# Optimization experiments

Measured on AMD Instinct MI355X. Metric: run time of the kernel, lower is better.

Reference implementation:

```python
import jax, jax.numpy as jnp
import numpy as np

B, H, L, D, S = 4, 16, 4096, 64, 128

def setup_inputs() -> dict:
    key = jax.random.key(0)
    k1, k2 = jax.random.split(key)
    x = jax.random.normal(k1, (B, H, L, D), dtype=jnp.float32)
    c = jax.random.normal(k2, (H, S, D), dtype=jnp.float32)
    # codebook rows are unit-normalized at init (matches torch init)
    c = c / jnp.linalg.norm(c, axis=-1, keepdims=True)
    return {"x": x, "c": c}

def reference(x, c):
    # cosine-similarity scores: [B,H,L,S]
    cos_sim = jnp.einsum('bhld,hsd->bhls', x, c)
    delta_index = jnp.argmax(cos_sim, axis=-1)            # [B,H,L]
    delta_onehot = jax.nn.one_hot(delta_index, c.shape[-2], dtype=jnp.float32)  # [B,H,L,S]
    return (delta_onehot, c)
```

## Files before the change

### kernel.cpp

```cpp
#include <hip/hip_runtime.h>
#include <math.h>

constexpr int BB = 4;
constexpr int HH = 16;
constexpr int LL = 4096;
constexpr int DD = 64;
constexpr int SS = 128;
constexpr int BM = 128;
constexpr int GG = 2;

constexpr float TAU = 2e-3f;

typedef __attribute__((ext_vector_type(8))) short bf16x8;
typedef __attribute__((ext_vector_type(4))) float f32x4;

#define MFMA16 __builtin_amdgcn_mfma_f32_16x16x32_bf16

__device__ __forceinline__ unsigned short f2bf(float v) {
    unsigned u = __float_as_uint(v);
    return (unsigned short)((u + 0x7fffu + ((u >> 16) & 1u)) >> 16);
}

__device__ __forceinline__ void split8(const float4 va, const float4 vb,
                                       uint4* hi, uint4* lo) {
    const float v[8] = {va.x, va.y, va.z, va.w, vb.x, vb.y, vb.z, vb.w};
    unsigned hw[4], lw[4];
    #pragma unroll
    for (int p = 0; p < 4; ++p) {
        const unsigned u0 = __float_as_uint(v[2 * p]);
        const unsigned u1 = __float_as_uint(v[2 * p + 1]);
        const unsigned h0 = u0 & 0xffff0000u;
        const unsigned h1 = u1 & 0xffff0000u;
        hw[p] = (u0 >> 16) | h1;
        lw[p] = (unsigned)f2bf(v[2 * p] - __uint_as_float(h0))
              | ((unsigned)f2bf(v[2 * p + 1] - __uint_as_float(h1)) << 16);
    }
    *hi = make_uint4(hw[0], hw[1], hw[2], hw[3]);
    *lo = make_uint4(lw[0], lw[1], lw[2], lw[3]);
}

union FragU { uint4 q; bf16x8 v; };

__global__ __launch_bounds__(256) void convert_c_kernel(
    const float* __restrict__ c, unsigned char* __restrict__ ws,
    float* __restrict__ out_c)
{
    const int sid = blockIdx.x * 256 + threadIdx.x;
    const int h  = sid >> 10;
    const int r  = sid & 1023;
    const int kt = r >> 9;
    const int ct = (r >> 6) & 7;
    const int ln = r & 63;
    const int cc = ct * 16 + (ln & 15);
    const int k0 = kt * 32 + (ln >> 4) * 8;
    const float4* src = (const float4*)(c + ((size_t)h * SS + cc) * DD + k0);
    uint4 hi, lo;
    split8(src[0], src[1], &hi, &lo);
    unsigned char* base =
        ws + (size_t)h * 32768 + (size_t)(((kt << 3) | ct) * 1024 + ln * 16);
    *(uint4*)(base) = hi;
    *(uint4*)(base + 16384) = lo;

    const f32x4* __restrict__ s4 = (const f32x4*)c;
    f32x4* __restrict__ d4 = (f32x4*)out_c;
    __builtin_nontemporal_store(s4[sid], d4 + sid);
    __builtin_nontemporal_store(s4[sid + 16384], d4 + sid + 16384);
}

__device__ __forceinline__ void load_a(const float* __restrict__ x,
                                       long long rbase, int wv, int lane,
                                       float4* raw) {
    const int ln15 = lane & 15;
    const int k0 = (lane >> 4) * 8;
    #pragma unroll
    for (int rtb = 0; rtb < 2; ++rtb) {
        const float* xr =
            x + (size_t)(rbase + wv * 32 + rtb * 16 + ln15) * DD + k0;
        #pragma unroll
        for (int kt = 0; kt < 2; ++kt) {
            raw[rtb * 4 + kt * 2 + 0] = *(const float4*)(xr + kt * 32);
            raw[rtb * 4 + kt * 2 + 1] = *(const float4*)(xr + kt * 32 + 4);
        }
    }
}

__device__ __forceinline__ void split_a(const float4* raw, bf16x8 af[2][2][2]) {
    #pragma unroll
    for (int rtb = 0; rtb < 2; ++rtb)
        #pragma unroll
        for (int kt = 0; kt < 2; ++kt) {
            FragU hi, lo;
            split8(raw[rtb * 4 + kt * 2], raw[rtb * 4 + kt * 2 + 1],
                   &hi.q, &lo.q);
            af[rtb][kt][0] = hi.v;
            af[rtb][kt][1] = lo.v;
        }
}

template <bool USE_WS>
__global__ __launch_bounds__(256, 2) void quantizer_kernel(
    const float* __restrict__ x,
    const float* __restrict__ c,
    const unsigned char* __restrict__ ws,
    float* __restrict__ out,
    float* __restrict__ out_c)
{
    __shared__ __align__(16) unsigned char smemB[32768];
    __shared__ int amax[GG][BM];
    __shared__ int s_wcnt[4];
    __shared__ int s_wlist[4][32];

    const int tid = threadIdx.x;
    const int wv = tid >> 6;
    const int lane = tid & 63;
    const int ln15 = lane & 15;
    const int blk = blockIdx.x;
    const long long base0 = (long long)blk * (GG * BM);
    const int h = (int)((base0 >> 12) & (HH - 1));
    const float* __restrict__ chead = c + (size_t)h * SS * DD;

    if (USE_WS) {
        const unsigned char* wsb = ws + (size_t)h * 32768;
        #pragma unroll
        for (int it = 0; it < 8; ++it) {
            const unsigned off = (unsigned)(wv * 8192 + it * 1024);
            __builtin_amdgcn_global_load_lds(
                (const __attribute__((address_space(1))) unsigned*)
                    (wsb + off + (unsigned)(lane * 16)),
                (__attribute__((address_space(3))) unsigned*)(smemB + off),
                16, 0, 0);
        }
    } else {
        #pragma unroll
        for (int it = 0; it < 4; ++it) {
            const int sid = it * 256 + tid;
            const int kt = sid >> 9;
            const int ct = (sid >> 6) & 7;
            const int ln = sid & 63;
            const int cc = ct * 16 + (ln & 15);
            const int k0 = kt * 32 + (ln >> 4) * 8;
            const float4* src = (const float4*)(chead + (size_t)cc * DD + k0);
            uint4 hi, lo;
            split8(src[0], src[1], &hi, &lo);
            unsigned char* dst = smemB + ((kt << 3) | ct) * 1024 + ln * 16;
            *(uint4*)dst = hi;
            *(uint4*)(dst + 16384) = lo;
        }
    }

    float4 xraw[8];
    load_a(x, base0, wv, lane, xraw);
    bf16x8 af[2][2][2];
    split_a(xraw, af);

    __syncthreads();

    #pragma unroll
    for (int g = 0; g < GG; ++g) {
        const long long rg = base0 + (long long)g * BM;
        int* __restrict__ amaxg = amax[g];

        if (lane == 0) s_wcnt[wv] = 0;

        if (g + 1 < GG) load_a(x, base0 + (long long)(g + 1) * BM,
                               wv, lane, xraw);

        float m1[2][4], m2[2][4];
        int   mi_[2][4];
        #pragma unroll
        for (int rtb = 0; rtb < 2; ++rtb)
            #pragma unroll
            for (int r = 0; r < 4; ++r) {
                m1[rtb][r] = -INFINITY; m2[rtb][r] = -INFINITY;
                mi_[rtb][r] = 0;
            }

        #pragma unroll
        for (int ct = 0; ct < 8; ++ct) {
            const unsigned bb = (unsigned)(ct << 10) + (unsigned)(lane * 16);
            const bf16x8 b10 = *(const bf16x8*)(smemB + bb);
            const bf16x8 b11 = *(const bf16x8*)(smemB + bb + 8192);
            const bf16x8 b20 = *(const bf16x8*)(smemB + bb + 16384);
            const bf16x8 b21 = *(const bf16x8*)(smemB + bb + 24576);
            #pragma unroll
            for (int rtb = 0; rtb < 2; ++rtb) {
                f32x4 a0 = {0.f, 0.f, 0.f, 0.f};
                f32x4 a1 = {0.f, 0.f, 0.f, 0.f};
                a0 = MFMA16(af[rtb][0][1], b10, a0, 0, 0, 0);
                a0 = MFMA16(af[rtb][0][0], b20, a0, 0, 0, 0);
                a0 = MFMA16(af[rtb][0][0], b10, a0, 0, 0, 0);
                a1 = MFMA16(af[rtb][1][1], b11, a1, 0, 0, 0);
                a1 = MFMA16(af[rtb][1][0], b21, a1, 0, 0, 0);
                a1 = MFMA16(af[rtb][1][0], b11, a1, 0, 0, 0);
                #pragma unroll
                for (int r = 0; r < 4; ++r) {
                    const float v = a0[r] + a1[r];
                    const int col = ct * 16 + ln15;
                    m2[rtb][r] =
                        __builtin_amdgcn_fmed3f(m1[rtb][r], v, m2[rtb][r]);
                    if (v > m1[rtb][r]) { m1[rtb][r] = v; mi_[rtb][r] = col; }
                }
            }
        }

        #pragma unroll
        for (int rtb = 0; rtb < 2; ++rtb) {
            #pragma unroll
            for (int r = 0; r < 4; ++r) {
                float a1 = m1[rtb][r], a2 = m2[rtb][r];
                int ai = mi_[rtb][r];
                #pragma unroll
                for (int off = 1; off <= 8; off <<= 1) {
                    const float o1 = __shfl_xor(a1, off);
                    const float o2 = __shfl_xor(a2, off);
                    const int   oi = __shfl_xor(ai, off);
                    const bool take = (o1 > a1) || (o1 == a1 && oi < ai);
                    const float n2 = take ? fmaxf(a1, o2) : fmaxf(a2, o1);
                    if (take) { a1 = o1; ai = oi; }
                    a2 = n2;
                }
                if (ln15 == 0) {
                    const int row = (2 * wv + rtb) * 16 + (lane >> 4) * 4 + r;
                    if (a1 - a2 >= TAU) {
                        amaxg[row] = ai;
                    } else {
                        const int p = atomicAdd(&s_wcnt[wv], 1);
                        s_wlist[wv][p] = row;
                    }
                }
            }
        }

        const int cnt = s_wcnt[wv];
        for (int f = 0; f < cnt; ++f) {
            const int row = s_wlist[wv][f];
            const float4* __restrict__ xr =
                (const float4*)(x + (size_t)(rg + row) * DD);
            const float4* __restrict__ c0 =
                (const float4*)(chead + (size_t)lane * DD);
            const float4* __restrict__ c1 =
                (const float4*)(chead + (size_t)(lane + 64) * DD);
            float s0 = 0.f, s1 = 0.f;
            #pragma unroll
            for (int q = 0; q < 16; ++q) {
                const float4 a = xr[q];
                const float4 b0 = c0[q];
                const float4 b1 = c1[q];
                s0 = fmaf(a.x, b0.x, s0); s0 = fmaf(a.y, b0.y, s0);
                s0 = fmaf(a.z, b0.z, s0); s0 = fmaf(a.w, b0.w, s0);
                s1 = fmaf(a.x, b1.x, s1); s1 = fmaf(a.y, b1.y, s1);
                s1 = fmaf(a.z, b1.z, s1); s1 = fmaf(a.w, b1.w, s1);
            }
            float v = s0; int bi = lane;
            if (s1 > v) { v = s1; bi = lane + 64; }
            #pragma unroll
            for (int off = 1; off < 64; off <<= 1) {
                const float ov = __shfl_xor(v, off);
                const int   oi = __shfl_xor(bi, off);
                if (ov > v || (ov == v && oi < bi)) { v = ov; bi = oi; }
            }
            if (lane == 0) amaxg[row] = bi;
        }
        __syncthreads();

        f32x4* __restrict__ op = (f32x4*)(out + (size_t)rg * SS);
        #pragma unroll 4
        for (int i = tid; i < BM * (SS / 4); i += 256) {
            const int rr = i >> 5;
            const int s0 = (i & 31) * 4;
            const int am = amaxg[rr];
            f32x4 v = {(s0 + 0 == am) ? 1.f : 0.f,
                       (s0 + 1 == am) ? 1.f : 0.f,
                       (s0 + 2 == am) ? 1.f : 0.f,
                       (s0 + 3 == am) ? 1.f : 0.f};
            __builtin_nontemporal_store(v, op + i);
        }

        if (g + 1 < GG) split_a(xraw, af);
    }

    if (!USE_WS && blk < 128) {
        const float4* __restrict__ src = (const float4*)c;
        float4* __restrict__ dst = (float4*)out_c;
        const int idx = blk * 256 + tid;
        dst[idx] = src[idx];
    }
}

extern "C" void kernel_launch(void* const* d_in, const int* in_sizes, int n_in,
                              void* d_out, int out_size, void* d_ws, size_t ws_size,
                              hipStream_t stream) {
    const float* x = (const float*)d_in[0];
    const float* c = (const float*)d_in[1];
    float* out = (float*)d_out;
    float* out_c = out + (size_t)BB * HH * LL * SS;

    const int rows = BB * HH * LL;
    const int blocks = rows / (GG * BM);
    const size_t ws_need = (size_t)HH * 32768;

    if (d_ws != nullptr && ws_size >= ws_need) {
        convert_c_kernel<<<64, 256, 0, stream>>>(c, (unsigned char*)d_ws,
                                                 out_c);
        quantizer_kernel<true><<<blocks, 256, 0, stream>>>(
            x, c, (const unsigned char*)d_ws, out, out_c);
    } else {
        quantizer_kernel<false><<<blocks, 256, 0, stream>>>(
            x, c, nullptr, out, out_c);
    }
}
```

Before: 202.1 us.

## Split fused quantizer into separate score and one-hot write kernels

The fused quantizer is split in two. A score kernel computes the argmax per row and writes it as int indices to a workspace buffer, and a separate onehot kernel then streams the large one-hot output. The intent is to take the bandwidth-heavy write phase away from the MFMA-heavy scoring phase, so each kernel can run at its own occupancy, and to drop the two-group loop. This adds a kernel launch and a small round trip through global memory for the indices. The per-block codebook load and x reload are no longer amortized over two groups.

```diff
diff --git a/kernel.cpp b/kernel.cpp
--- a/kernel.cpp
+++ b/kernel.cpp
@@ -7,7 +7,6 @@
 constexpr int DD = 64;
 constexpr int SS = 128;
 constexpr int BM = 128;
-constexpr int GG = 2;
 
 constexpr float TAU = 2e-3f;
 
@@ -97,16 +96,14 @@
         }
 }
 
-template <bool USE_WS>
-__global__ __launch_bounds__(256, 2) void quantizer_kernel(
+__global__ __launch_bounds__(256, 2) void score_kernel(
     const float* __restrict__ x,
     const float* __restrict__ c,
     const unsigned char* __restrict__ ws,
-    float* __restrict__ out,
-    float* __restrict__ out_c)
+    int* __restrict__ amax_g)
 {
     __shared__ __align__(16) unsigned char smemB[32768];
-    __shared__ int amax[GG][BM];
+    __shared__ int s_res[4][32];
     __shared__ int s_wcnt[4];
     __shared__ int s_wlist[4][32];
 
@@ -114,12 +111,13 @@
     const int wv = tid >> 6;
     const int lane = tid & 63;
     const int ln15 = lane & 15;
-    const int blk = blockIdx.x;
-    const long long base0 = (long long)blk * (GG * BM);
-    const int h = (int)((base0 >> 12) & (HH - 1));
+    const long long r0 = (long long)blockIdx.x * BM;
+    const int h = (int)((r0 >> 12) & (HH - 1));
     const float* __restrict__ chead = c + (size_t)h * SS * DD;
 
-    if (USE_WS) {
+    if (lane == 0) s_wcnt[wv] = 0;
+
+    {
         const unsigned char* wsb = ws + (size_t)h * 32768;
         #pragma unroll
         for (int it = 0; it < 8; ++it) {
@@ -130,156 +128,292 @@
                 (__attribute__((address_space(3))) unsigned*)(smemB + off),
                 16, 0, 0);
         }
-    } else {
-        #pragma unroll
-        for (int it = 0; it < 4; ++it) {
-            const int sid = it * 256 + tid;
-            const int kt = sid >> 9;
-            const int ct = (sid >> 6) & 7;
-            const int ln = sid & 63;
-            const int cc = ct * 16 + (ln & 15);
-            const int k0 = kt * 32 + (ln >> 4) * 8;
-            const float4* src = (const float4*)(chead + (size_t)cc * DD + k0);
-            uint4 hi, lo;
-            split8(src[0], src[1], &hi, &lo);
-            unsigned char* dst = smemB + ((kt << 3) | ct) * 1024 + ln * 16;
-            *(uint4*)dst = hi;
-            *(uint4*)(dst + 16384) = lo;
-        }
     }
 
     float4 xraw[8];
-    load_a(x, base0, wv, lane, xraw);
+    load_a(x, r0, wv, lane, xraw);
     bf16x8 af[2][2][2];
     split_a(xraw, af);
 
     __syncthreads();
 
-    #pragma unroll
-    for (int g = 0; g < GG; ++g) {
-        const long long rg = base0 + (long long)g * BM;
-        int* __restrict__ amaxg = amax[g];
-
-        if (lane == 0) s_wcnt[wv] = 0;
-
-        if (g + 1 < GG) load_a(x, base0 + (long long)(g + 1) * BM,
-                               wv, lane, xraw);
-
-        float m1[2][4], m2[2][4];
-        int   mi_[2][4];
-        #pragma unroll
-        for (int rtb = 0; rtb < 2; ++rtb)
+    float m1[2][4], m2[2][4];
+    int   mi_[2][4];
+    #pragma unroll
+    for (int rtb = 0; rtb < 2; ++rtb)
+        #pragma unroll
+        for (int r = 0; r < 4; ++r) {
+            m1[rtb][r] = -INFINITY; m2[rtb][r] = -INFINITY; mi_[rtb][r] = 0;
+        }
+
+    #pragma unroll
+    for (int ct = 0; ct < 8; ++ct) {
+        const unsigned bb = (unsigned)(ct << 10) + (unsigned)(lane * 16);
+        const bf16x8 b10 = *(const bf16x8*)(smemB + bb);
+        const bf16x8 b11 = *(const bf16x8*)(smemB + bb + 8192);
+        const bf16x8 b20 = *(const bf16x8*)(smemB + bb + 16384);
+        const bf16x8 b21 = *(const bf16x8*)(smemB + bb + 24576);
+        #pragma unroll
+        for (int rtb = 0; rtb < 2; ++rtb) {
+            f32x4 a0 = {0.f, 0.f, 0.f, 0.f};
+            f32x4 a1 = {0.f, 0.f, 0.f, 0.f};
+            a0 = MFMA16(af[rtb][0][1], b10, a0, 0, 0, 0);
+            a0 = MFMA16(af[rtb][0][0], b20, a0, 0, 0, 0);
+            a0 = MFMA16(af[rtb][0][0], b10, a0, 0, 0, 0);
+            a1 = MFMA16(af[rtb][1][1], b11, a1, 0, 0, 0);
+            a1 = MFMA16(af[rtb][1][0], b21, a1, 0, 0, 0);
+            a1 = MFMA16(af[rtb][1][0], b11, a1, 0, 0, 0);
             #pragma unroll
             for (int r = 0; r < 4; ++r) {
-                m1[rtb][r] = -INFINITY; m2[rtb][r] = -INFINITY;
-                mi_[rtb][r] = 0;
-            }
-
-        #pragma unroll
-        for (int ct = 0; ct < 8; ++ct) {
-            const unsigned bb = (unsigned)(ct << 10) + (unsigned)(lane * 16);
-            const bf16x8 b10 = *(const bf16x8*)(smemB + bb);
-            const bf16x8 b11 = *(const bf16x8*)(smemB + bb + 8192);
-            const bf16x8 b20 = *(const bf16x8*)(smemB + bb + 16384);
-            const bf16x8 b21 = *(const bf16x8*)(smemB + bb + 24576);
+                const float v = a0[r] + a1[r];
+                const int col = ct * 16 + ln15;
+                m2[rtb][r] = __builtin_amdgcn_fmed3f(m1[rtb][r], v, m2[rtb][r]);
+                if (v > m1[rtb][r]) { m1[rtb][r] = v; mi_[rtb][r] = col; }
+            }
+        }
+    }
+
+    #pragma unroll
+    for (int rtb = 0; rtb < 2; ++rtb) {
+        int rv[4];
+        #pragma unroll
+        for (int r = 0; r < 4; ++r) {
+            float a1 = m1[rtb][r], a2 = m2[rtb][r];
+            int ai = mi_[rtb][r];
             #pragma unroll
-            for (int rtb = 0; rtb < 2; ++rtb) {
-                f32x4 a0 = {0.f, 0.f, 0.f, 0.f};
-                f32x4 a1 = {0.f, 0.f, 0.f, 0.f};
-                a0 = MFMA16(af[rtb][0][1], b10, a0, 0, 0, 0);
-                a0 = MFMA16(af[rtb][0][0], b20, a0, 0, 0, 0);
-                a0 = MFMA16(af[rtb][0][0], b10, a0, 0, 0, 0);
-                a1 = MFMA16(af[rtb][1][1], b11, a1, 0, 0, 0);
-                a1 = MFMA16(af[rtb][1][0], b21, a1, 0, 0, 0);
-                a1 = MFMA16(af[rtb][1][0], b11, a1, 0, 0, 0);
-                #pragma unroll
-                for (int r = 0; r < 4; ++r) {
-                    const float v = a0[r] + a1[r];
-                    const int col = ct * 16 + ln15;
-                    m2[rtb][r] =
-                        __builtin_amdgcn_fmed3f(m1[rtb][r], v, m2[rtb][r]);
-                    if (v > m1[rtb][r]) { m1[rtb][r] = v; mi_[rtb][r] = col; }
-                }
-            }
-        }
-
+            for (int off = 1; off <= 8; off <<= 1) {
+                const float o1 = __shfl_xor(a1, off);
+                const float o2 = __shfl_xor(a2, off);
+                const int   oi = __shfl_xor(ai, off);
+                const bool take = (o1 > a1) || (o1 == a1 && oi < ai);
+                const float n2 = take ? fmaxf(a1, o2) : fmaxf(a2, o1);
+                if (take) { a1 = o1; ai = oi; }
+                a2 = n2;
+            }
+            rv[r] = ai;
+            if (ln15 == 0 && (a1 - a2) < TAU) {
+                const int p = atomicAdd(&s_wcnt[wv], 1);
+                s_wlist[wv][p] = rtb * 16 + (lane >> 4) * 4 + r;
+            }
+        }
+        if (ln15 == 0)
+            *(int4*)&s_res[wv][rtb * 16 + (lane >> 4) * 4] =
+                make_int4(rv[0], rv[1], rv[2], rv[3]);
+    }
+
+    const int cnt = s_wcnt[wv];
+    for (int f = 0; f < cnt; ++f) {
+        const int local = s_wlist[wv][f];
+        const float4* __restrict__ xr =
+            (const float4*)(x + (size_t)(r0 + wv * 32 + local) * DD);
+        const float4* __restrict__ c0 =
+            (const float4*)(chead + (size_t)lane * DD);
+        const float4* __restrict__ c1 =
+            (const float4*)(chead + (size_t)(lane + 64) * DD);
+        float s0 = 0.f, s1 = 0.f;
+        #pragma unroll
+        for (int q = 0; q < 16; ++q) {
+            const float4 a = xr[q];
+            const float4 b0 = c0[q];
+            const float4 b1 = c1[q];
+            s0 = fmaf(a.x, b0.x, s0); s0 = fmaf(a.y, b0.y, s0);
+            s0 = fmaf(a.z, b0.z, s0); s0 = fmaf(a.w, b0.w, s0);
+            s1 = fmaf(a.x, b1.x, s1); s1 = fmaf(a.y, b1.y, s1);
+            s1 = fmaf(a.z, b1.z, s1); s1 = fmaf(a.w, b1.w, s1);
+        }
+        float v = s0; int bi = lane;
+        if (s1 > v) { v = s1; bi = lane + 64; }
+        #pragma unroll
+        for (int off = 1; off < 64; off <<= 1) {
+            const float ov = __shfl_xor(v, off);
+            const int   oi = __shfl_xor(bi, off);
+            if (ov > v || (ov == v && oi < bi)) { v = ov; bi = oi; }
+        }
+        if (lane == 0) s_res[wv][local] = bi;
+    }
+
+    if (lane < 8) {
+        const int4 v = ((const int4*)s_res[wv])[lane];
+        *(int4*)(amax_g + r0 + wv * 32 + lane * 4) = v;
+    }
+}
+
+__global__ __launch_bounds__(256) void onehot_kernel(
+    const int* __restrict__ amax_g, float* __restrict__ out)
+{
+    __shared__ int sA[BM];
+    const int tid = threadIdx.x;
+    const long long r0 = (long long)blockIdx.x * BM;
+    if (tid < 32)
+        ((int4*)sA)[tid] = *(const int4*)(amax_g + r0 + tid * 4);
+    __syncthreads();
+
+    f32x4* __restrict__ op = (f32x4*)(out + (size_t)r0 * SS);
+    #pragma unroll
+    for (int k = 0; k < 16; ++k) {
+        const int i = tid + k * 256;
+        const int am = sA[i >> 5];
+        const int s0 = (i & 31) * 4;
+        f32x4 v = {(s0 + 0 == am) ? 1.f : 0.f,
+                   (s0 + 1 == am) ? 1.f : 0.f,
+                   (s0 + 2 == am) ? 1.f : 0.f,
+                   (s0 + 3 == am) ? 1.f : 0.f};
+        __builtin_nontemporal_store(v, op + i);
+    }
+}
+
+__global__ __launch_bounds__(256, 2) void quantizer_fused(
+    const float* __restrict__ x, const float* __restrict__ c,
+    float* __restrict__ out, float* __restrict__ out_c)
+{
+    __shared__ __align__(16) unsigned char smemB[32768];
+    __shared__ int amax[BM];
+    __shared__ int s_wcnt[4];
+    __shared__ int s_wlist[4][32];
+
+    const int tid = threadIdx.x;
+    const int wv = tid >> 6;
+    const int lane = tid & 63;
+    const int ln15 = lane & 15;
+    const int blk = blockIdx.x;
+    const long long r0 = (long long)blk * BM;
+    const int h = (int)((r0 >> 12) & (HH - 1));
+    const float* __restrict__ chead = c + (size_t)h * SS * DD;
+
+    if (lane == 0) s_wcnt[wv] = 0;
+
+    #pragma unroll
+    for (int it = 0; it < 4; ++it) {
+        const int sid = it * 256 + tid;
+        const int kt = sid >> 9;
+        const int ct = (sid >> 6) & 7;
+        const int ln = sid & 63;
+        const int cc = ct * 16 + (ln & 15);
+        const int k0 = kt * 32 + (ln >> 4) * 8;
+        const float4* src = (const float4*)(chead + (size_t)cc * DD + k0);
+        uint4 hi, lo;
+        split8(src[0], src[1], &hi, &lo);
+        unsigned char* dst = smemB + ((kt << 3) | ct) * 1024 + ln * 16;
+        *(uint4*)dst = hi;
+        *(uint4*)(dst + 16384) = lo;
+    }
+
+    float4 xraw[8];
+    load_a(x, r0, wv, lane, xraw);
+    bf16x8 af[2][2][2];
+    split_a(xraw, af);
+    __syncthreads();
+
+    float m1[2][4], m2[2][4];
+    int   mi_[2][4];
+    #pragma unroll
+    for (int rtb = 0; rtb < 2; ++rtb)
+        #pragma unroll
+        for (int r = 0; r < 4; ++r) {
+            m1[rtb][r] = -INFINITY; m2[rtb][r] = -INFINITY; mi_[rtb][r] = 0;
+        }
+
+    #pragma unroll
+    for (int ct = 0; ct < 8; ++ct) {
+        const unsigned bb = (unsigned)(ct << 10) + (unsigned)(lane * 16);
+        const bf16x8 b10 = *(const bf16x8*)(smemB + bb);
+        const bf16x8 b11 = *(const bf16x8*)(smemB + bb + 8192);
+        const bf16x8 b20 = *(const bf16x8*)(smemB + bb + 16384);
+        const bf16x8 b21 = *(const bf16x8*)(smemB + bb + 24576);
         #pragma unroll
         for (int rtb = 0; rtb < 2; ++rtb) {
+            f32x4 a0 = {0.f, 0.f, 0.f, 0.f};
+            f32x4 a1 = {0.f, 0.f, 0.f, 0.f};
+            a0 = MFMA16(af[rtb][0][1], b10, a0, 0, 0, 0);
+            a0 = MFMA16(af[rtb][0][0], b20, a0, 0, 0, 0);
+            a0 = MFMA16(af[rtb][0][0], b10, a0, 0, 0, 0);
+            a1 = MFMA16(af[rtb][1][1], b11, a1, 0, 0, 0);
+            a1 = MFMA16(af[rtb][1][0], b21, a1, 0, 0, 0);
+            a1 = MFMA16(af[rtb][1][0], b11, a1, 0, 0, 0);
             #pragma unroll
             for (int r = 0; r < 4; ++r) {
-                float a1 = m1[rtb][r], a2 = m2[rtb][r];
-                int ai = mi_[rtb][r];
-                #pragma unroll
-                for (int off = 1; off <= 8; off <<= 1) {
-                    const float o1 = __shfl_xor(a1, off);
-                    const float o2 = __shfl_xor(a2, off);
-                    const int   oi = __shfl_xor(ai, off);
-                    const bool take = (o1 > a1) || (o1 == a1 && oi < ai);
-                    const float n2 = take ? fmaxf(a1, o2) : fmaxf(a2, o1);
-                    if (take) { a1 = o1; ai = oi; }
-                    a2 = n2;
+                const float v = a0[r] + a1[r];
+                const int col = ct * 16 + ln15;
+                m2[rtb][r] = __builtin_amdgcn_fmed3f(m1[rtb][r], v, m2[rtb][r]);
+                if (v > m1[rtb][r]) { m1[rtb][r] = v; mi_[rtb][r] = col; }
+            }
+        }
+    }
+
+    #pragma unroll
+    for (int rtb = 0; rtb < 2; ++rtb) {
+        #pragma unroll
+        for (int r = 0; r < 4; ++r) {
+            float a1 = m1[rtb][r], a2 = m2[rtb][r];
+            int ai = mi_[rtb][r];
+            #pragma unroll
+            for (int off = 1; off <= 8; off <<= 1) {
+                const float o1 = __shfl_xor(a1, off);
+                const float o2 = __shfl_xor(a2, off);
+                const int   oi = __shfl_xor(ai, off);
+                const bool take = (o1 > a1) || (o1 == a1 && oi < ai);
+                const float n2 = take ? fmaxf(a1, o2) : fmaxf(a2, o1);
+                if (take) { a1 = o1; ai = oi; }
+                a2 = n2;
+            }
+            if (ln15 == 0) {
+                const int row = (2 * wv + rtb) * 16 + (lane >> 4) * 4 + r;
+                if (a1 - a2 >= TAU) {
+                    amax[row] = ai;
+                } else {
+                    const int p = atomicAdd(&s_wcnt[wv], 1);
+                    s_wlist[wv][p] = row;
                 }
-                if (ln15 == 0) {
-                    const int row = (2 * wv + rtb) * 16 + (lane >> 4) * 4 + r;
-                    if (a1 - a2 >= TAU) {
-                        amaxg[row] = ai;
-                    } else {
-                        const int p = atomicAdd(&s_wcnt[wv], 1);
-                        s_wlist[wv][p] = row;
-                    }
-                }
-            }
-        }
-
-        const int cnt = s_wcnt[wv];
-        for (int f = 0; f < cnt; ++f) {
-            const int row = s_wlist[wv][f];
-            const float4* __restrict__ xr =
-                (const float4*)(x + (size_t)(rg + row) * DD);
-            const float4* __restrict__ c0 =
-                (const float4*)(chead + (size_t)lane * DD);
-            const float4* __restrict__ c1 =
-                (const float4*)(chead + (size_t)(lane + 64) * DD);
-            float s0 = 0.f, s1 = 0.f;
-            #pragma unroll
-            for (int q = 0; q < 16; ++q) {
-                const float4 a = xr[q];
-                const float4 b0 = c0[q];
-                const float4 b1 = c1[q];
-                s0 = fmaf(a.x, b0.x, s0); s0 = fmaf(a.y, b0.y, s0);
-                s0 = fmaf(a.z, b0.z, s0); s0 = fmaf(a.w, b0.w, s0);
-                s1 = fmaf(a.x, b1.x, s1); s1 = fmaf(a.y, b1.y, s1);
-                s1 = fmaf(a.z, b1.z, s1); s1 = fmaf(a.w, b1.w, s1);
-            }
-            float v = s0; int bi = lane;
-            if (s1 > v) { v = s1; bi = lane + 64; }
-            #pragma unroll
-            for (int off = 1; off < 64; off <<= 1) {
-                const float ov = __shfl_xor(v, off);
-                const int   oi = __shfl_xor(bi, off);
-                if (ov > v || (ov == v && oi < bi)) { v = ov; bi = oi; }
-            }
-            if (lane == 0) amaxg[row] = bi;
-        }
-        __syncthreads();
-
-        f32x4* __restrict__ op = (f32x4*)(out + (size_t)rg * SS);
-        #pragma unroll 4
-        for (int i = tid; i < BM * (SS / 4); i += 256) {
-            const int rr = i >> 5;
-            const int s0 = (i & 31) * 4;
-            const int am = amaxg[rr];
-            f32x4 v = {(s0 + 0 == am) ? 1.f : 0.f,
-                       (s0 + 1 == am) ? 1.f : 0.f,
-                       (s0 + 2 == am) ? 1.f : 0.f,
-                       (s0 + 3 == am) ? 1.f : 0.f};
-            __builtin_nontemporal_store(v, op + i);
-        }
-
-        if (g + 1 < GG) split_a(xraw, af);
-    }
-
-    if (!USE_WS && blk < 128) {
+            }
+        }
+    }
+
+    const int cnt = s_wcnt[wv];
+    for (int f = 0; f < cnt; ++f) {
+        const int row = s_wlist[wv][f];
+        const float4* __restrict__ xr =
+            (const float4*)(x + (size_t)(r0 + row) * DD);
+        const float4* __restrict__ c0 =
+            (const float4*)(chead + (size_t)lane * DD);
+        const float4* __restrict__ c1 =
+            (const float4*)(chead + (size_t)(lane + 64) * DD);
+        float s0 = 0.f, s1 = 0.f;
+        #pragma unroll
+        for (int q = 0; q < 16; ++q) {
+            const float4 a = xr[q];
+            const float4 b0 = c0[q];
+            const float4 b1 = c1[q];
+            s0 = fmaf(a.x, b0.x, s0); s0 = fmaf(a.y, b0.y, s0);
+            s0 = fmaf(a.z, b0.z, s0); s0 = fmaf(a.w, b0.w, s0);
+            s1 = fmaf(a.x, b1.x, s1); s1 = fmaf(a.y, b1.y, s1);
+            s1 = fmaf(a.z, b1.z, s1); s1 = fmaf(a.w, b1.w, s1);
+        }
+        float v = s0; int bi = lane;
+        if (s1 > v) { v = s1; bi = lane + 64; }
+        #pragma unroll
+        for (int off = 1; off < 64; off <<= 1) {
+            const float ov = __shfl_xor(v, off);
+            const int   oi = __shfl_xor(bi, off);
+            if (ov > v || (ov == v && oi < bi)) { v = ov; bi = oi; }
+        }
+        if (lane == 0) amax[row] = bi;
+    }
+    __syncthreads();
+
+    f32x4* __restrict__ op = (f32x4*)(out + (size_t)r0 * SS);
+    #pragma unroll 4
+    for (int i = tid; i < BM * (SS / 4); i += 256) {
+        const int rr = i >> 5;
+        const int s0 = (i & 31) * 4;
+        const int am = amax[rr];
+        f32x4 v = {(s0 + 0 == am) ? 1.f : 0.f,
+                   (s0 + 1 == am) ? 1.f : 0.f,
+                   (s0 + 2 == am) ? 1.f : 0.f,
+                   (s0 + 3 == am) ? 1.f : 0.f};
+        __builtin_nontemporal_store(v, op + i);
+    }
+
+    if (blk < 128) {
         const float4* __restrict__ src = (const float4*)c;
         float4* __restrict__ dst = (float4*)out_c;
         const int idx = blk * 256 + tid;
@@ -296,16 +430,17 @@
     float* out_c = out + (size_t)BB * HH * LL * SS;
 
     const int rows = BB * HH * LL;
-    const int blocks = rows / (GG * BM);
-    const size_t ws_need = (size_t)HH * 32768;
+    const int blocks = rows / BM;
+    const size_t wsB_bytes = (size_t)HH * 32768;
+    const size_t ws_need = wsB_bytes + (size_t)rows * 4;
 
     if (d_ws != nullptr && ws_size >= ws_need) {
-        convert_c_kernel<<<64, 256, 0, stream>>>(c, (unsigned char*)d_ws,
-                                                 out_c);
-        quantizer_kernel<true><<<blocks, 256, 0, stream>>>(
-            x, c, (const unsigned char*)d_ws, out, out_c);
+        unsigned char* wsB = (unsigned char*)d_ws;
+        int* amax_g = (int*)(wsB + wsB_bytes);
+        convert_c_kernel<<<64, 256, 0, stream>>>(c, wsB, out_c);
+        score_kernel<<<blocks, 256, 0, stream>>>(x, c, wsB, amax_g);
+        onehot_kernel<<<blocks, 256, 0, stream>>>(amax_g, out);
     } else {
-        quantizer_kernel<false><<<blocks, 256, 0, stream>>>(
-            x, c, nullptr, out, out_c);
-    }
-}
+        quantizer_fused<<<blocks, 256, 0, stream>>>(x, c, out, out_c);
+    }
+}
```

After: 208.8 us. 3.3% more time.

## Make argmax and one-hot write per-wave, dropping block barrier; double rows per block

Applied to the files above, without the earlier changes.

Each wave now stores its own 32 row argmax results in a per-wave shared buffer and writes the one-hot rows for those rows itself. This removes the block-wide __syncthreads between the argmax phase and the output-write phase. Rows per block go from 256 to 512 (GG 2→4), halving the grid and spreading the codebook staging cost over more rows. The risk is fewer blocks for occupancy and possible reuse hazards on s_wcnt/s_res across groups, since there is no barrier between iterations.

```diff
diff --git a/kernel.cpp b/kernel.cpp
--- a/kernel.cpp
+++ b/kernel.cpp
@@ -7,7 +7,7 @@
 constexpr int DD = 64;
 constexpr int SS = 128;
 constexpr int BM = 128;
-constexpr int GG = 2;
+constexpr int GG = 4;
 
 constexpr float TAU = 2e-3f;
 
@@ -106,7 +106,7 @@
     float* __restrict__ out_c)
 {
     __shared__ __align__(16) unsigned char smemB[32768];
-    __shared__ int amax[GG][BM];
+    __shared__ int s_res[4][32];
     __shared__ int s_wcnt[4];
     __shared__ int s_wlist[4][32];
 
@@ -114,9 +114,8 @@
     const int wv = tid >> 6;
     const int lane = tid & 63;
     const int ln15 = lane & 15;
-    const int blk = blockIdx.x;
-    const long long base0 = (long long)blk * (GG * BM);
-    const int h = (int)((base0 >> 12) & (HH - 1));
+    const long long R0 = (long long)blockIdx.x * (GG * BM);
+    const int h = (int)((R0 >> 12) & (HH - 1));
     const float* __restrict__ chead = c + (size_t)h * SS * DD;
 
     if (USE_WS) {
@@ -149,7 +148,7 @@
     }
 
     float4 xraw[8];
-    load_a(x, base0, wv, lane, xraw);
+    load_a(x, R0, wv, lane, xraw);
     bf16x8 af[2][2][2];
     split_a(xraw, af);
 
@@ -157,13 +156,11 @@
 
     #pragma unroll
     for (int g = 0; g < GG; ++g) {
-        const long long rg = base0 + (long long)g * BM;
-        int* __restrict__ amaxg = amax[g];
+        const long long rg = R0 + (long long)g * BM;
 
         if (lane == 0) s_wcnt[wv] = 0;
 
-        if (g + 1 < GG) load_a(x, base0 + (long long)(g + 1) * BM,
-                               wv, lane, xraw);
+        if (g + 1 < GG) load_a(x, rg + BM, wv, lane, xraw);
 
         float m1[2][4], m2[2][4];
         int   mi_[2][4];
@@ -205,6 +202,7 @@
 
         #pragma unroll
         for (int rtb = 0; rtb < 2; ++rtb) {
+            int rv[4];
             #pragma unroll
             for (int r = 0; r < 4; ++r) {
                 float a1 = m1[rtb][r], a2 = m2[rtb][r];
@@ -219,23 +217,22 @@
                     if (take) { a1 = o1; ai = oi; }
                     a2 = n2;
                 }
-                if (ln15 == 0) {
-                    const int row = (2 * wv + rtb) * 16 + (lane >> 4) * 4 + r;
-                    if (a1 - a2 >= TAU) {
-                        amaxg[row] = ai;
-                    } else {
-                        const int p = atomicAdd(&s_wcnt[wv], 1);
-                        s_wlist[wv][p] = row;
-                    }
+                rv[r] = ai;
+                if (ln15 == 0 && (a1 - a2) < TAU) {
+                    const int p = atomicAdd(&s_wcnt[wv], 1);
+                    s_wlist[wv][p] = rtb * 16 + (lane >> 4) * 4 + r;
                 }
             }
+            if (ln15 == 0)
+                *(int4*)&s_res[wv][rtb * 16 + (lane >> 4) * 4] =
+                    make_int4(rv[0], rv[1], rv[2], rv[3]);
         }
 
         const int cnt = s_wcnt[wv];
         for (int f = 0; f < cnt; ++f) {
-            const int row = s_wlist[wv][f];
+            const int local = s_wlist[wv][f];
             const float4* __restrict__ xr =
-                (const float4*)(x + (size_t)(rg + row) * DD);
+                (const float4*)(x + (size_t)(rg + wv * 32 + local) * DD);
             const float4* __restrict__ c0 =
                 (const float4*)(chead + (size_t)lane * DD);
             const float4* __restrict__ c1 =
@@ -259,16 +256,16 @@
                 const int   oi = __shfl_xor(bi, off);
                 if (ov > v || (ov == v && oi < bi)) { v = ov; bi = oi; }
             }
-            if (lane == 0) amaxg[row] = bi;
-        }
-        __syncthreads();
-
-        f32x4* __restrict__ op = (f32x4*)(out + (size_t)rg * SS);
-        #pragma unroll 4
-        for (int i = tid; i < BM * (SS / 4); i += 256) {
-            const int rr = i >> 5;
+            if (lane == 0) s_res[wv][local] = bi;
+        }
+
+        f32x4* __restrict__ op =
+            (f32x4*)(out + (size_t)(rg + wv * 32) * SS);
+        #pragma unroll
+        for (int k = 0; k < 16; ++k) {
+            const int i = lane + k * 64;
+            const int am = s_res[wv][i >> 5];
             const int s0 = (i & 31) * 4;
-            const int am = amaxg[rr];
             f32x4 v = {(s0 + 0 == am) ? 1.f : 0.f,
                        (s0 + 1 == am) ? 1.f : 0.f,
                        (s0 + 2 == am) ? 1.f : 0.f,
@@ -279,10 +276,10 @@
         if (g + 1 < GG) split_a(xraw, af);
     }
 
-    if (!USE_WS && blk < 128) {
+    if (!USE_WS && blockIdx.x < 128) {
         const float4* __restrict__ src = (const float4*)c;
         float4* __restrict__ dst = (float4*)out_c;
-        const int idx = blk * 256 + tid;
+        const int idx = blockIdx.x * 256 + tid;
         dst[idx] = src[idx];
     }
 }
```

Result: slower. 259.5 us (+28.4%).
